# Performance work log

Measured on AMD Instinct MI355X. Metric: run time of the kernel, lower is better.

The kernel has to match this reference:

```python
import jax, jax.numpy as jnp
import numpy as np

B, F_, D, DIM, HEADS, DH = 1, 16, 576, 320, 8, 40
INNER = HEADS * DH          # 320
CROSS, TLEN = 768, 77
FF_INNER = 4 * DIM          # 1280
EPS = 1e-5


def _ln(x, w, b):
    mu = jnp.mean(x, axis=-1, keepdims=True)
    var = jnp.mean(jnp.square(x - mu), axis=-1, keepdims=True)
    return (x - mu) * jax.lax.rsqrt(var + EPS) * w + b


def _mha(q, k, v, heads):
    # q: [n, sq, inner], k/v: [n, sk, inner]
    n, sq, inner = q.shape
    sk = k.shape[1]
    dh = inner // heads
    q = q.reshape(n, sq, heads, dh).transpose(0, 2, 1, 3)
    k = k.reshape(n, sk, heads, dh).transpose(0, 2, 1, 3)
    v = v.reshape(n, sk, heads, dh).transpose(0, 2, 1, 3)
    scores = jnp.einsum('nhqd,nhkd->nhqk', q, k) * (dh ** -0.5)
    probs = jax.nn.softmax(scores, axis=-1)
    out = jnp.einsum('nhqk,nhkd->nhqd', probs, v)
    return out.transpose(0, 2, 1, 3).reshape(n, sq, inner)


def setup_inputs():
    key = jax.random.key(0)
    ks = jax.random.split(key, 32)
    s = 0.02

    def W(k, shape):
        return jax.random.normal(k, shape, jnp.float32) * s

    return {
        'hidden_states': jax.random.normal(ks[0], (B * F_, D, DIM), jnp.float32),
        'encoder_hidden_states': jax.random.normal(ks[1], (B * F_, TLEN, CROSS), jnp.float32),
        'ln1_w': jnp.ones((DIM,)), 'ln1_b': jnp.zeros((DIM,)),
        'q1_w': W(ks[2], (DIM, INNER)), 'k1_w': W(ks[3], (DIM, INNER)), 'v1_w': W(ks[4], (DIM, INNER)),
        'o1_w': W(ks[5], (INNER, DIM)), 'o1_b': jnp.zeros((DIM,)),
        'ln2_w': jnp.ones((DIM,)), 'ln2_b': jnp.zeros((DIM,)),
        'q2_w': W(ks[6], (DIM, INNER)), 'k2_w': W(ks[7], (CROSS, INNER)), 'v2_w': W(ks[8], (CROSS, INNER)),
        'o2_w': W(ks[9], (INNER, DIM)), 'o2_b': jnp.zeros((DIM,)),
        'lnt_w': jnp.ones((DIM,)), 'lnt_b': jnp.zeros((DIM,)),
        'qt_w': W(ks[10], (DIM, INNER)), 'kt_w': W(ks[11], (DIM, INNER)), 'vt_w': W(ks[12], (DIM, INNER)),
        'ot_w': W(ks[13], (INNER, DIM)), 'ot_b': jnp.zeros((DIM,)),
        'ln3_w': jnp.ones((DIM,)), 'ln3_b': jnp.zeros((DIM,)),
        'geglu_w': W(ks[14], (DIM, 2 * FF_INNER)), 'geglu_b': jnp.zeros((2 * FF_INNER,)),
        'ffo_w': W(ks[15], (FF_INNER, DIM)), 'ffo_b': jnp.zeros((DIM,)),
        'video_length': F_,
    }


def reference(hidden_states, encoder_hidden_states,
              ln1_w, ln1_b, q1_w, k1_w, v1_w, o1_w, o1_b,
              ln2_w, ln2_b, q2_w, k2_w, v2_w, o2_w, o2_b,
              lnt_w, lnt_b, qt_w, kt_w, vt_w, ot_w, ot_b,
              ln3_w, ln3_b, geglu_w, geglu_b, ffo_w, ffo_b,
              video_length):
    bf, d, c = hidden_states.shape
    f = video_length
    b = bf // f

    # ---- 1. sparse-causal self attention ----
    norm = _ln(hidden_states, ln1_w, ln1_b)
    q = norm @ q1_w
    k = (norm @ k1_w).reshape(b, f, d, INNER)
    v = (norm @ v1_w).reshape(b, f, d, INNER)
    former = jnp.clip(jnp.arange(f) - 1, 0, None)  # former_frame_index, [0,0,1,...]
    first = jnp.broadcast_to(k[:, :1], (b, f, d, INNER))
    k = jnp.concatenate([first, k[:, former]], axis=2).reshape(bf, 2 * d, INNER)
    firstv = jnp.broadcast_to(v[:, :1], (b, f, d, INNER))
    v = jnp.concatenate([firstv, v[:, former]], axis=2).reshape(bf, 2 * d, INNER)
    attn1 = _mha(q, k, v, HEADS) @ o1_w + o1_b
    hidden_states = attn1 + hidden_states

    # ---- 2. cross attention ----
    norm = _ln(hidden_states, ln2_w, ln2_b)
    attn2 = _mha(norm @ q2_w, encoder_hidden_states @ k2_w,
                 encoder_hidden_states @ v2_w, HEADS) @ o2_w + o2_b
    hidden_states = attn2 + hidden_states

    # ---- 3. temporal attention: (b f) d c -> (b d) f c ----
    ht = hidden_states.reshape(b, f, d, c).transpose(0, 2, 1, 3).reshape(b * d, f, c)
    norm = _ln(ht, lnt_w, lnt_b)
    attn_t = _mha(norm @ qt_w, norm @ kt_w, norm @ vt_w, HEADS) @ ot_w + ot_b
    ht = attn_t + ht
    hidden_states = ht.reshape(b, d, f, c).transpose(0, 2, 1, 3).reshape(bf, d, c)

    # ---- 4. GEGLU feed-forward ----
    norm = _ln(hidden_states, ln3_w, ln3_b)
    proj = norm @ geglu_w + geglu_b
    x1, gate = jnp.split(proj, 2, axis=-1)
    ff = (x1 * jax.nn.gelu(gate, approximate=False)) @ ffo_w + ffo_b
    return ff + hidden_states
```

## Files before the change

### kernel.cpp

```cpp
#include <hip/hip_runtime.h>
#include <hip/hip_bf16.h>
#include <math.h>

typedef unsigned short u16;
typedef unsigned int   u32;
typedef __attribute__((ext_vector_type(4))) float f32x4;
typedef __attribute__((ext_vector_type(8))) short bf8;
typedef __attribute__((ext_vector_type(4))) short bf4;

#define DEV __device__ __forceinline__

constexpr int FRAMES = 16, DTOK = 576, CDIM = 320, NHEAD = 8, DH = 40;
constexpr int TOKS = FRAMES * DTOK;
constexpr int TLEN = 77;
constexpr int FFI  = 1280;

constexpr int FP = 68;

DEV float b2f(u16 u) { union { u32 i; float f; } v; v.i = ((u32)u) << 16; return v.f; }
DEV u16 f2b(float f) {
  union { float f; u32 i; } v; v.f = f;
  return (u16)((v.i + 0x7fffu + ((v.i >> 16) & 1u)) >> 16);
}
DEV u32 cvtpk(float lo, float hi) {
  u32 r;
  asm("v_cvt_pk_bf16_f32 %0, %1, %2" : "=v"(r) : "v"(lo), "v"(hi));
  return r;
}

DEV bf8 ldfrag(const u16* p) {
  bf4 lo = *(const bf4*)p;
  bf4 hi = *(const bf4*)(p + 16);
  bf8 r;
  r[0]=lo[0]; r[1]=lo[1]; r[2]=lo[2]; r[3]=lo[3];
  r[4]=hi[0]; r[5]=hi[1]; r[6]=hi[2]; r[7]=hi[3];
  return r;
}

DEV f32x4 mfma16(bf8 a, bf8 b, f32x4 c) {
  return __builtin_amdgcn_mfma_f32_16x16x32_bf16(a, b, c, 0, 0, 0);
}

struct TD { const float* src; u16* dst; int K; int N; };
struct TPack { TD d[15]; };

__global__ __launch_bounds__(256) void tr_k(TPack p) {
  TD t = p.d[blockIdx.y];
  int total = t.K * t.N;
  for (int i = blockIdx.x * 256 + threadIdx.x; i < total; i += gridDim.x * 256) {
    int k = i / t.N, n = i % t.N;
    t.dst[(long)n * t.K + k] = f2b(t.src[i]);
  }
}

__global__ __launch_bounds__(256)
void ln_k(const float* __restrict__ X, const float* __restrict__ wt,
          const float* __restrict__ bs, u16* __restrict__ out) {
  const int row  = blockIdx.x * 4 + (threadIdx.x >> 6);
  const int lane = threadIdx.x & 63;
  const long base = (long)row * CDIM;
  float v[5];
#pragma unroll
  for (int i = 0; i < 5; i++) v[i] = X[base + i * 64 + lane];
  float s = v[0] + v[1] + v[2] + v[3] + v[4];
#pragma unroll
  for (int d = 1; d < 64; d <<= 1) s += __shfl_xor(s, d);
  const float mu = s * (1.0f / 320.0f);
  float dv[5], q = 0.f;
#pragma unroll
  for (int i = 0; i < 5; i++) { dv[i] = v[i] - mu; q += dv[i] * dv[i]; }
#pragma unroll
  for (int d = 1; d < 64; d <<= 1) q += __shfl_xor(q, d);
  const float rs = rsqrtf(q * (1.0f / 320.0f) + 1e-5f);
#pragma unroll
  for (int i = 0; i < 5; i++) {
    int c = i * 64 + lane;
    out[base + c] = f2b(dv[i] * rs * wt[c] + bs[c]);
  }
}

template<int MODE>
__global__ __launch_bounds__(256)
void gemm_k(const u16* __restrict__ A,
            const u16* __restrict__ Ba, const u16* __restrict__ Bb,
            const u16* __restrict__ Bc,
            u16* oa, u16* ob, u16* oc,
            const float* __restrict__ bias, const float* __restrict__ bias2,
            const float* __restrict__ resf, float* __restrict__ outf,
            int M, int N, int K, float oscale) {
  int bx, by, bz;
  {
    const int gx = gridDim.x, gy = gridDim.y, gz = gridDim.z;
    const int nwg = gx * gy * gz;
    int flat = blockIdx.x + gx * (blockIdx.y + gy * blockIdx.z);
    int orig = ((nwg & 7) == 0) ? (flat & 7) * (nwg >> 3) + (flat >> 3) : flat;
    bz = orig % gz;
    int rem = orig / gz;
    bx = rem % gx;
    by = rem / gx;
  }

  const u16* BT; u16* outb;
  if (MODE == 2) { BT = Ba; outb = oa; }
  else {
    BT   = (bz == 0) ? Ba : (bz == 1 ? Bb : Bc);
    outb = (bz == 0) ? oa : (bz == 1 ? ob : oc);
  }
  const u16* BT2 = Bb;
  const float zscale = (MODE == 0 && bz == 0) ? oscale : 1.0f;

  __shared__ __align__(16) u16 As[2][128][FP];
  __shared__ __align__(16) u16 Bs[2][64][FP];
  __shared__ __align__(16) u16 Bs2[(MODE == 2) ? 2 : 1][(MODE == 2) ? 64 : 1][(MODE == 2) ? FP : 1];

  const int tid = threadIdx.x;
  const int lane = tid & 63, w = tid >> 6;
  const int lr = lane & 15, lg = lane >> 4;
  const int wr = w >> 1, wc = w & 1;
  const long bm = (long)by * 128;
  const int  bn = bx * 64;

  f32x4 acc[4][2];
  f32x4 acc2[(MODE == 2) ? 4 : 1][(MODE == 2) ? 2 : 1];
  const f32x4 z4 = {0.f, 0.f, 0.f, 0.f};
#pragma unroll
  for (int f = 0; f < 4; f++)
#pragma unroll
    for (int g = 0; g < 2; g++) { acc[f][g] = z4; if (MODE == 2) acc2[f][g] = z4; }

  const int  arow = tid >> 1, aseg = tid & 1;
  const long agr  = bm + arow;
  const int  brow = tid >> 2, bseg = tid & 3;
  const bf8  zv   = {0,0,0,0,0,0,0,0};

  bf8 aReg[4], bReg[2], bReg2[(MODE == 2) ? 2 : 1];
  auto prefetch = [&](int k0) {
    const u16* asrc = A + agr * K + k0 + aseg * 32;
    if (agr < M) {
#pragma unroll
      for (int i = 0; i < 4; i++) aReg[i] = *(const bf8*)(asrc + i * 8);
    } else {
#pragma unroll
      for (int i = 0; i < 4; i++) aReg[i] = zv;
    }
    const u16* bsrc = BT + (long)(bn + brow) * K + k0 + bseg * 16;
    bReg[0] = *(const bf8*)(bsrc);
    bReg[1] = *(const bf8*)(bsrc + 8);
    if (MODE == 2) {
      const u16* bsrc2 = BT2 + (long)(bn + brow) * K + k0 + bseg * 16;
      bReg2[0] = *(const bf8*)(bsrc2);
      bReg2[1] = *(const bf8*)(bsrc2 + 8);
    }
  };
  auto writeLDS = [&](int buf) {
#pragma unroll
    for (int i = 0; i < 4; i++)
      *(bf8*)&As[buf][arow][aseg * 32 + i * 8] = aReg[i];
    *(bf8*)&Bs[buf][brow][bseg * 16]     = bReg[0];
    *(bf8*)&Bs[buf][brow][bseg * 16 + 8] = bReg[1];
    if (MODE == 2) {
      *(bf8*)&Bs2[buf][brow][bseg * 16]     = bReg2[0];
      *(bf8*)&Bs2[buf][brow][bseg * 16 + 8] = bReg2[1];
    }
  };

  prefetch(0);
  writeLDS(0);
  if (K > 64) prefetch(64);

  int cur = 0;
  for (int k0 = 0; k0 < K; k0 += 64) {
    asm volatile("s_waitcnt lgkmcnt(0)" ::: "memory");
    __builtin_amdgcn_s_barrier();

#pragma unroll
    for (int kk = 0; kk < 64; kk += 32) {
      bf8 af[4], bfr[2], bfr2[2];
#pragma unroll
      for (int f = 0; f < 4; f++)
        af[f] = ldfrag(&As[cur][wr * 64 + f * 16 + lr][kk + lg * 4]);
#pragma unroll
      for (int g = 0; g < 2; g++)
        bfr[g] = ldfrag(&Bs[cur][wc * 32 + g * 16 + lr][kk + lg * 4]);
      if (MODE == 2) {
#pragma unroll
        for (int g = 0; g < 2; g++)
          bfr2[g] = ldfrag(&Bs2[cur][wc * 32 + g * 16 + lr][kk + lg * 4]);
      }
#pragma unroll
      for (int f = 0; f < 4; f++)
#pragma unroll
        for (int g = 0; g < 2; g++) {
          acc[f][g] = mfma16(af[f], bfr[g], acc[f][g]);
          if (MODE == 2) acc2[f][g] = mfma16(af[f], bfr2[g], acc2[f][g]);
        }
    }

    if (k0 + 64 < K) {
      writeLDS(cur ^ 1);
      if (k0 + 128 < K) prefetch(k0 + 128);
    }
    cur ^= 1;
  }

#pragma unroll
  for (int f = 0; f < 4; f++)
#pragma unroll
    for (int g = 0; g < 2; g++)
#pragma unroll
      for (int j = 0; j < 4; j++) {
        long gm = bm + wr * 64 + f * 16 + lg * 4 + j;
        if (gm >= M) continue;
        int gn = bn + wc * 32 + g * 16 + lr;
        long o = gm * N + gn;
        float v = acc[f][g][j];
        if (MODE == 0) outb[o] = f2b(v * zscale);
        if (MODE == 1) outf[o] = v + bias[gn] + resf[o];
        if (MODE == 2) {
          float x1 = v + bias[gn];
          float gt = acc2[f][g][j] + bias2[gn];
          float ge = 0.5f * gt * (1.0f + erff(gt * 0.70710678118f));
          outb[o] = f2b(x1 * ge);
        }
      }
}

template<int MODE>
__global__ __launch_bounds__(256)
void flash_k(const u16* __restrict__ Q, const u16* __restrict__ Kb,
             const u16* __restrict__ Vb, u16* __restrict__ O) {
  __shared__ __align__(16) u16 Ks[2][64][FP];
  __shared__ __align__(16) u16 Vt[2][48][FP];
  u16 (*Qs)[FP] = Ks[1];

  int qb, h, n;
  {
    int flat = blockIdx.x + 9 * (blockIdx.y + 8 * blockIdx.z);
    int orig = (flat & 7) * 144 + (flat >> 3);
    qb = orig % 9; int rem = orig / 9;
    h = rem & 7; n = rem >> 3;
  }
  const int tid = threadIdx.x, lane = tid & 63, w = tid >> 6;
  const int lr = lane & 15, lg = lane >> 4;
  const int hoff = h * DH;

  constexpr int NCH   = (MODE == 0) ? 18 : 2;
  constexpr int KVLEN = (MODE == 0) ? 2 * DTOK : TLEN;
  const int nch = (MODE == 0 && n == 0) ? 9 : NCH;
  const int fprev = (n == 0) ? 0 : n - 1;
  const u16* Kh = Kb + hoff;
  const u16* Vh = Vb + hoff;

  int rS[5], cS[5]; long off[5];
#pragma unroll
  for (int j = 0; j < 5; j++) {
    int e = tid + j * 256;
    rS[j] = e / 20; cS[j] = (e % 20) * 2;
    off[j] = (long)rS[j] * CDIM + cS[j];
  }

  u32 kreg[5], vreg[5];
  auto prefetch = [&](int cc) {
    if (MODE == 0) {
      const long rowbase = (cc < 9) ? (long)cc * 64
                                    : (long)fprev * DTOK + (cc - 9) * 64;
      const u16* kp = Kh + rowbase * CDIM;
      const u16* vp = Vh + rowbase * CDIM;
#pragma unroll
      for (int j = 0; j < 5; j++) {
        kreg[j] = *(const u32*)(kp + off[j]);
        vreg[j] = *(const u32*)(vp + off[j]);
      }
    } else {
#pragma unroll
      for (int j = 0; j < 5; j++) {
        int t = cc * 64 + rS[j];
        bool valid = t < TLEN;
        long o = ((long)n * TLEN + t) * CDIM + cS[j];
        kreg[j] = valid ? *(const u32*)(Kh + o) : 0u;
        vreg[j] = valid ? *(const u32*)(Vh + o) : 0u;
      }
    }
  };
  auto writeKV = [&](int buf) {
#pragma unroll
    for (int j = 0; j < 5; j++) *(u32*)&Ks[buf][rS[j]][cS[j]] = kreg[j];
#pragma unroll
    for (int j = 0; j < 5; j++) {
      Vt[buf][cS[j]][rS[j]]     = (u16)(vreg[j] & 0xffffu);
      Vt[buf][cS[j] + 1][rS[j]] = (u16)(vreg[j] >> 16);
    }
  };

  prefetch(0);

  for (int i = tid; i < 64 * 24; i += 256) {
    int r = i / 24, c = 40 + (i % 24);
    Ks[0][r][c] = 0; Ks[1][r][c] = 0;
  }
  for (int i = tid; i < 8 * 64; i += 256) {
    int r = 40 + (i >> 6), c = i & 63;
    u16 pv = (r == 40) ? (u16)0x3F80 : (u16)0;
    Vt[0][r][c] = pv; Vt[1][r][c] = pv;
  }

  const int qrow0 = n * DTOK + qb * 64;
  for (int i = tid; i < 64 * 20; i += 256) {
    int r = i / 20, cp = (i % 20) * 2;
    *(u32*)&Qs[r][cp] = *(const u32*)(Q + (long)(qrow0 + r) * CDIM + hoff + cp);
  }
  writeKV(0);
  if (nch > 1) prefetch(1);
  asm volatile("s_waitcnt lgkmcnt(0)" ::: "memory");
  __builtin_amdgcn_s_barrier();

  bf8 qf[2];
  {
    const u16* p = &Qs[w * 16 + lr][0];
    qf[0] = ldfrag(p + lg * 4);
    qf[1] = ldfrag(p + 32 + lg * 4);
  }
  asm volatile("s_waitcnt lgkmcnt(0)" ::: "memory");
  __builtin_amdgcn_s_barrier();

  f32x4 oacc[3];
  const f32x4 z4 = {0.f, 0.f, 0.f, 0.f};
#pragma unroll
  for (int g = 0; g < 3; g++) oacc[g] = z4;

  int cur = 0;

  for (int cc = 0; cc < nch; cc++) {
    f32x4 s[4];
#pragma unroll
    for (int nf = 0; nf < 4; nf++) {
      const u16* kp = &Ks[cur][nf * 16 + lr][0];
      bf8 k0 = ldfrag(kp + lg * 4);
      bf8 k1 = ldfrag(kp + 32 + lg * 4);
      f32x4 z = z4;
      z = mfma16(k0, qf[0], z);
      z = mfma16(k1, qf[1], z);
      s[nf] = z;
    }

    float pvv[16];
#pragma unroll
    for (int nf = 0; nf < 4; nf++)
#pragma unroll
      for (int j = 0; j < 4; j++) {
        float p = exp2f(s[nf][j]);
        if (MODE == 1) {
          int kv = cc * 64 + nf * 16 + lg * 4 + j;
          if (kv >= KVLEN) p = 0.f;
        }
        pvv[nf * 4 + j] = p;
      }
    union { u32 u[4]; bf8 v; } P0, P1;
#pragma unroll
    for (int k2 = 0; k2 < 4; k2++) {
      P0.u[k2] = cvtpk(pvv[2 * k2],     pvv[2 * k2 + 1]);
      P1.u[k2] = cvtpk(pvv[8 + 2 * k2], pvv[8 + 2 * k2 + 1]);
    }
    bf8 pf0 = P0.v, pf1 = P1.v;

#pragma unroll
    for (int g = 0; g < 3; g++) {
      const u16* vp = &Vt[cur][g * 16 + lr][0];
      bf8 v0 = ldfrag(vp + lg * 4);
      bf8 v1 = ldfrag(vp + 32 + lg * 4);
      oacc[g] = mfma16(pf0, v0, oacc[g]);
      oacc[g] = mfma16(pf1, v1, oacc[g]);
    }

    if (cc + 1 < nch) {
      writeKV(cur ^ 1);
      if (cc + 2 < nch) prefetch(cc + 2);
      asm volatile("s_waitcnt lgkmcnt(0)" ::: "memory");
      __builtin_amdgcn_s_barrier();
    }
    cur ^= 1;
  }

  float lsum[4];
#pragma unroll
  for (int j = 0; j < 4; j++)
    lsum[j] = __shfl(oacc[2][j], (lane & 0x30) + 8);

#pragma unroll
  for (int g = 0; g < 3; g++) {
    int col = g * 16 + lr;
    if (col < DH) {
#pragma unroll
      for (int j = 0; j < 4; j++) {
        long row = qrow0 + w * 16 + lg * 4 + j;
        O[row * CDIM + hoff + col] = f2b(oacc[g][j] / lsum[j]);
      }
    }
  }
}

__global__ __launch_bounds__(64)
void tattn_k(const u16* __restrict__ Q, const u16* __restrict__ Kb,
             const u16* __restrict__ Vb, u16* __restrict__ O) {
  const int d = blockIdx.x, h = blockIdx.y;
  const int lane = threadIdx.x;
  __shared__ float Qs[16][41], Ks[16][41], Vs[16][41], Ps[16][17];
  const int hoff = h * DH;
#pragma unroll
  for (int i = 0; i < 10; i++) {
    int e = lane + 64 * i;
    int t = e / 40, c = e % 40;
    long src = (long)(t * DTOK + d) * CDIM + hoff + c;
    Qs[t][c] = b2f(Q[src]); Ks[t][c] = b2f(Kb[src]); Vs[t][c] = b2f(Vb[src]);
  }
  __syncthreads();
  const int ki = lane & 15, qg = lane >> 4;
  float p[4];
#pragma unroll
  for (int j = 0; j < 4; j++) {
    int qi = qg * 4 + j;
    float s = 0.f;
#pragma unroll
    for (int c = 0; c < 40; c++) s += Qs[qi][c] * Ks[ki][c];
    p[j] = s;
  }
#pragma unroll
  for (int j = 0; j < 4; j++) {
    float mx = p[j];
#pragma unroll
    for (int dd = 1; dd < 16; dd <<= 1) mx = fmaxf(mx, __shfl_xor(mx, dd));
    float e = exp2f(p[j] - mx);
    float ss = e;
#pragma unroll
    for (int dd = 1; dd < 16; dd <<= 1) ss += __shfl_xor(ss, dd);
    Ps[qg * 4 + j][ki] = e / ss;
  }
  __syncthreads();
  const int qi2 = lane & 15, dg = lane >> 4;
#pragma unroll
  for (int mI = 0; mI < 10; mI++) {
    int dd = dg * 10 + mI;
    float o = 0.f;
#pragma unroll
    for (int k2 = 0; k2 < 16; k2++) o += Ps[qi2][k2] * Vs[k2][dd];
    O[(long)(qi2 * DTOK + d) * CDIM + hoff + dd] = f2b(o);
  }
}

extern "C" void kernel_launch(void* const* d_in, const int* in_sizes, int n_in,
                              void* d_out, int out_size, void* d_ws, size_t ws_size,
                              hipStream_t stream) {
  const float* hid  = (const float*)d_in[0];
  const float* enc  = (const float*)d_in[1];
  const float* ln1w = (const float*)d_in[2];  const float* ln1b = (const float*)d_in[3];
  const float* q1w  = (const float*)d_in[4];  const float* k1w  = (const float*)d_in[5];
  const float* v1w  = (const float*)d_in[6];  const float* o1w  = (const float*)d_in[7];
  const float* o1b  = (const float*)d_in[8];
  const float* ln2w = (const float*)d_in[9];  const float* ln2b = (const float*)d_in[10];
  const float* q2w  = (const float*)d_in[11]; const float* k2w  = (const float*)d_in[12];
  const float* v2w  = (const float*)d_in[13]; const float* o2w  = (const float*)d_in[14];
  const float* o2b  = (const float*)d_in[15];
  const float* lntw = (const float*)d_in[16]; const float* lntb = (const float*)d_in[17];
  const float* qtw  = (const float*)d_in[18]; const float* ktw  = (const float*)d_in[19];
  const float* vtw  = (const float*)d_in[20]; const float* otw  = (const float*)d_in[21];
  const float* otb  = (const float*)d_in[22];
  const float* ln3w = (const float*)d_in[23]; const float* ln3b = (const float*)d_in[24];
  const float* gegw = (const float*)d_in[25]; const float* gegb = (const float*)d_in[26];
  const float* ffow = (const float*)d_in[27]; const float* ffob = (const float*)d_in[28];

  char* ws = (char*)d_ws;
  size_t off = 0;
  auto alloc = [&](size_t bytes) -> void* {
    void* p = ws + off;
    off = (off + bytes + 255) & ~(size_t)255;
    return p;
  };

  u16* wq1T = (u16*)alloc(320 * 320 * 2);
  u16* wk1T = (u16*)alloc(320 * 320 * 2);
  u16* wv1T = (u16*)alloc(320 * 320 * 2);
  u16* wo1T = (u16*)alloc(320 * 320 * 2);
  u16* wq2T = (u16*)alloc(320 * 320 * 2);
  u16* wk2T = (u16*)alloc(768 * 320 * 2);
  u16* wv2T = (u16*)alloc(768 * 320 * 2);
  u16* wo2T = (u16*)alloc(320 * 320 * 2);
  u16* wqtT = (u16*)alloc(320 * 320 * 2);
  u16* wktT = (u16*)alloc(320 * 320 * 2);
  u16* wvtT = (u16*)alloc(320 * 320 * 2);
  u16* wotT = (u16*)alloc(320 * 320 * 2);
  u16* wggT = (u16*)alloc(320 * 2560 * 2);
  u16* wfoT = (u16*)alloc(1280 * 320 * 2);

  u16*   ffin  = (u16*)alloc((size_t)TOKS * FFI * 2);
  u16* Qb    = ffin;
  u16* Kb    = ffin + (size_t)TOKS * CDIM;
  u16* Vb    = ffin + (size_t)2 * TOKS * CDIM;
  u16* attnB = ffin + (size_t)3 * TOKS * CDIM;
  u16*   normA = (u16*)alloc((size_t)TOKS * CDIM * 2);
  u16*   encB  = (u16*)alloc((size_t)16 * TLEN * 768 * 2);
  float* H1    = (float*)alloc((size_t)TOKS * CDIM * 4);
  float* H2    = (float*)alloc((size_t)TOKS * CDIM * 4);
  float* H3    = H1;

  if (off > ws_size) return;

  const int ENCN = 16 * TLEN * 768;
  TPack tp;
  tp.d[0]  = {q1w, wq1T, 320, 320};
  tp.d[1]  = {k1w, wk1T, 320, 320};
  tp.d[2]  = {v1w, wv1T, 320, 320};
  tp.d[3]  = {o1w, wo1T, 320, 320};
  tp.d[4]  = {q2w, wq2T, 320, 320};
  tp.d[5]  = {k2w, wk2T, 768, 320};
  tp.d[6]  = {v2w, wv2T, 768, 320};
  tp.d[7]  = {o2w, wo2T, 320, 320};
  tp.d[8]  = {qtw, wqtT, 320, 320};
  tp.d[9]  = {ktw, wktT, 320, 320};
  tp.d[10] = {vtw, wvtT, 320, 320};
  tp.d[11] = {otw, wotT, 320, 320};
  tp.d[12] = {gegw, wggT, 320, 2560};
  tp.d[13] = {ffow, wfoT, 1280, 320};
  tp.d[14] = {enc,  encB, 1, ENCN};

  const int MENC = 16 * TLEN;
  const float QS = 0.2281101122f;

  tr_k<<<dim3(320, 15), 256, 0, stream>>>(tp);

  ln_k<<<TOKS / 4, 256, 0, stream>>>(hid, ln1w, ln1b, normA);
  gemm_k<0><<<dim3(5, 72, 3), 256, 0, stream>>>(normA, wq1T, wk1T, wv1T,
      Qb, Kb, Vb, nullptr, nullptr, nullptr, nullptr, TOKS, 320, 320, QS);
  flash_k<0><<<dim3(9, 8, 16), 256, 0, stream>>>(Qb, Kb, Vb, attnB);
  gemm_k<1><<<dim3(5, 72, 1), 256, 0, stream>>>(attnB, wo1T, nullptr, nullptr,
      nullptr, nullptr, nullptr, o1b, nullptr, hid, H1, TOKS, 320, 320, 1.f);

  ln_k<<<TOKS / 4, 256, 0, stream>>>(H1, ln2w, ln2b, normA);
  gemm_k<0><<<dim3(5, 72, 1), 256, 0, stream>>>(normA, wq2T, nullptr, nullptr,
      Qb, nullptr, nullptr, nullptr, nullptr, nullptr, nullptr, TOKS, 320, 320, QS);
  gemm_k<0><<<dim3(5, 10, 2), 256, 0, stream>>>(encB, wk2T, wv2T, nullptr,
      Kb, Vb, nullptr, nullptr, nullptr, nullptr, nullptr, MENC, 320, 768, 1.f);
  flash_k<1><<<dim3(9, 8, 16), 256, 0, stream>>>(Qb, Kb, Vb, attnB);
  gemm_k<1><<<dim3(5, 72, 1), 256, 0, stream>>>(attnB, wo2T, nullptr, nullptr,
      nullptr, nullptr, nullptr, o2b, nullptr, H1, H2, TOKS, 320, 320, 1.f);

  ln_k<<<TOKS / 4, 256, 0, stream>>>(H2, lntw, lntb, normA);
  gemm_k<0><<<dim3(5, 72, 3), 256, 0, stream>>>(normA, wqtT, wktT, wvtT,
      Qb, Kb, Vb, nullptr, nullptr, nullptr, nullptr, TOKS, 320, 320, QS);
  tattn_k<<<dim3(576, 8), 64, 0, stream>>>(Qb, Kb, Vb, attnB);
  gemm_k<1><<<dim3(5, 72, 1), 256, 0, stream>>>(attnB, wotT, nullptr, nullptr,
      nullptr, nullptr, nullptr, otb, nullptr, H2, H3, TOKS, 320, 320, 1.f);

  ln_k<<<TOKS / 4, 256, 0, stream>>>(H3, ln3w, ln3b, normA);
  gemm_k<2><<<dim3(20, 72, 1), 256, 0, stream>>>(normA, wggT, wggT + 1280 * 320,
      nullptr, ffin, nullptr, nullptr, gegb, gegb + 1280, nullptr, nullptr,
      TOKS, 1280, 320, 1.f);
  gemm_k<1><<<dim3(5, 72, 1), 256, 0, stream>>>(ffin, wfoT, nullptr, nullptr,
      nullptr, nullptr, nullptr, ffob, nullptr, H3, (float*)d_out, TOKS, 320, 1280, 1.f);
}
```

Baseline: 290.7 us.

## Load K and Q fragments straight from global into registers in flash attention

Drops the shared-memory K buffer and the Q staging step. K fragments are now read from global memory straight into registers and double-buffered across a two-chunk unrolled loop, so the next chunk's K loads overlap the current chunk's MFMAs. Q fragments are loaded directly, with the padded tail zeroed in registers, which removes one barrier and the LDS writes for K. The cost is more VGPR pressure and narrow strided global reads. In cross-attention mode, K rows past the 77-token length are now read without a bounds guard and rely on masking, so the last batch item may read past the end of the buffer.

```diff
diff --git a/kernel.cpp b/kernel.cpp
--- a/kernel.cpp
+++ b/kernel.cpp
@@ -229,9 +229,7 @@
 __global__ __launch_bounds__(256)
 void flash_k(const u16* __restrict__ Q, const u16* __restrict__ Kb,
              const u16* __restrict__ Vb, u16* __restrict__ O) {
-  __shared__ __align__(16) u16 Ks[2][64][FP];
   __shared__ __align__(16) u16 Vt[2][48][FP];
-  u16 (*Qs)[FP] = Ks[1];
 
   int qb, h, n;
   {
@@ -259,32 +257,25 @@
     off[j] = (long)rS[j] * CDIM + cS[j];
   }
 
-  u32 kreg[5], vreg[5];
-  auto prefetch = [&](int cc) {
+  u32 vreg[5];
+  auto prefetchV = [&](int cc) {
     if (MODE == 0) {
       const long rowbase = (cc < 9) ? (long)cc * 64
                                     : (long)fprev * DTOK + (cc - 9) * 64;
-      const u16* kp = Kh + rowbase * CDIM;
       const u16* vp = Vh + rowbase * CDIM;
 #pragma unroll
-      for (int j = 0; j < 5; j++) {
-        kreg[j] = *(const u32*)(kp + off[j]);
-        vreg[j] = *(const u32*)(vp + off[j]);
-      }
+      for (int j = 0; j < 5; j++) vreg[j] = *(const u32*)(vp + off[j]);
     } else {
 #pragma unroll
       for (int j = 0; j < 5; j++) {
         int t = cc * 64 + rS[j];
         bool valid = t < TLEN;
         long o = ((long)n * TLEN + t) * CDIM + cS[j];
-        kreg[j] = valid ? *(const u32*)(Kh + o) : 0u;
         vreg[j] = valid ? *(const u32*)(Vh + o) : 0u;
       }
     }
   };
-  auto writeKV = [&](int buf) {
-#pragma unroll
-    for (int j = 0; j < 5; j++) *(u32*)&Ks[buf][rS[j]][cS[j]] = kreg[j];
+  auto writeV = [&](int buf) {
 #pragma unroll
     for (int j = 0; j < 5; j++) {
       Vt[buf][cS[j]][rS[j]]     = (u16)(vreg[j] & 0xffffu);
@@ -292,100 +283,108 @@
     }
   };
 
-  prefetch(0);
-
-  for (int i = tid; i < 64 * 24; i += 256) {
-    int r = i / 24, c = 40 + (i % 24);
-    Ks[0][r][c] = 0; Ks[1][r][c] = 0;
-  }
+  auto loadK = [&](int cc, bf8 (&k0)[4], bf8 (&k1)[4]) {
+    long rowbase;
+    if (MODE == 0)
+      rowbase = (cc < 9) ? (long)cc * 64 : (long)fprev * DTOK + (cc - 9) * 64;
+    else
+      rowbase = (long)n * TLEN + cc * 64;
+#pragma unroll
+    for (int nf = 0; nf < 4; nf++) {
+      const u16* kp = Kh + (rowbase + nf * 16 + lr) * CDIM + lg * 4;
+      k0[nf] = ldfrag(kp);
+      k1[nf] = ldfrag(kp + 32);
+    }
+  };
+
+  bf8 kA0[4], kA1[4], kB0[4], kB1[4];
+
+  prefetchV(0);
+  loadK(0, kA0, kA1);
+
+  bf8 qf0, qf1;
+  {
+    const u16* qp = Q + (long)(n * DTOK + qb * 64 + w * 16 + lr) * CDIM + hoff + lg * 4;
+    qf0 = ldfrag(qp);
+    bf4 lo = (lg < 2) ? *(const bf4*)(qp + 32) : bf4{0, 0, 0, 0};
+    qf1[0] = lo[0]; qf1[1] = lo[1]; qf1[2] = lo[2]; qf1[3] = lo[3];
+    qf1[4] = 0; qf1[5] = 0; qf1[6] = 0; qf1[7] = 0;
+  }
+
   for (int i = tid; i < 8 * 64; i += 256) {
     int r = 40 + (i >> 6), c = i & 63;
     u16 pv = (r == 40) ? (u16)0x3F80 : (u16)0;
     Vt[0][r][c] = pv; Vt[1][r][c] = pv;
   }
 
-  const int qrow0 = n * DTOK + qb * 64;
-  for (int i = tid; i < 64 * 20; i += 256) {
-    int r = i / 20, cp = (i % 20) * 2;
-    *(u32*)&Qs[r][cp] = *(const u32*)(Q + (long)(qrow0 + r) * CDIM + hoff + cp);
-  }
-  writeKV(0);
-  if (nch > 1) prefetch(1);
+  writeV(0);
+  if (nch > 1) prefetchV(1);
   asm volatile("s_waitcnt lgkmcnt(0)" ::: "memory");
   __builtin_amdgcn_s_barrier();
 
-  bf8 qf[2];
-  {
-    const u16* p = &Qs[w * 16 + lr][0];
-    qf[0] = ldfrag(p + lg * 4);
-    qf[1] = ldfrag(p + 32 + lg * 4);
-  }
-  asm volatile("s_waitcnt lgkmcnt(0)" ::: "memory");
-  __builtin_amdgcn_s_barrier();
-
   f32x4 oacc[3];
   const f32x4 z4 = {0.f, 0.f, 0.f, 0.f};
 #pragma unroll
   for (int g = 0; g < 3; g++) oacc[g] = z4;
 
-  int cur = 0;
-
-  for (int cc = 0; cc < nch; cc++) {
-    f32x4 s[4];
-#pragma unroll
-    for (int nf = 0; nf < 4; nf++) {
-      const u16* kp = &Ks[cur][nf * 16 + lr][0];
-      bf8 k0 = ldfrag(kp + lg * 4);
-      bf8 k1 = ldfrag(kp + 32 + lg * 4);
-      f32x4 z = z4;
-      z = mfma16(k0, qf[0], z);
-      z = mfma16(k1, qf[1], z);
-      s[nf] = z;
-    }
-
-    float pvv[16];
-#pragma unroll
-    for (int nf = 0; nf < 4; nf++)
-#pragma unroll
-      for (int j = 0; j < 4; j++) {
-        float p = exp2f(s[nf][j]);
-        if (MODE == 1) {
-          int kv = cc * 64 + nf * 16 + lg * 4 + j;
-          if (kv >= KVLEN) p = 0.f;
-        }
-        pvv[nf * 4 + j] = p;
-      }
-    union { u32 u[4]; bf8 v; } P0, P1;
-#pragma unroll
-    for (int k2 = 0; k2 < 4; k2++) {
-      P0.u[k2] = cvtpk(pvv[2 * k2],     pvv[2 * k2 + 1]);
-      P1.u[k2] = cvtpk(pvv[8 + 2 * k2], pvv[8 + 2 * k2 + 1]);
-    }
-    bf8 pf0 = P0.v, pf1 = P1.v;
-
-#pragma unroll
-    for (int g = 0; g < 3; g++) {
-      const u16* vp = &Vt[cur][g * 16 + lr][0];
-      bf8 v0 = ldfrag(vp + lg * 4);
-      bf8 v1 = ldfrag(vp + 32 + lg * 4);
-      oacc[g] = mfma16(pf0, v0, oacc[g]);
-      oacc[g] = mfma16(pf1, v1, oacc[g]);
-    }
-
-    if (cc + 1 < nch) {
-      writeKV(cur ^ 1);
-      if (cc + 2 < nch) prefetch(cc + 2);
-      asm volatile("s_waitcnt lgkmcnt(0)" ::: "memory");
-      __builtin_amdgcn_s_barrier();
-    }
-    cur ^= 1;
-  }
+#define CHUNK_BODY(CC, K0, K1, KN0, KN1, VB)                                  \
+  {                                                                           \
+    const int cc_ = (CC);                                                     \
+    if (cc_ + 1 < nch) loadK(cc_ + 1, KN0, KN1);                              \
+    f32x4 s[4];                                                               \
+    _Pragma("unroll")                                                         \
+    for (int nf = 0; nf < 4; nf++) {                                          \
+      f32x4 z = z4;                                                           \
+      z = mfma16(K0[nf], qf0, z);                                             \
+      z = mfma16(K1[nf], qf1, z);                                             \
+      s[nf] = z;                                                              \
+    }                                                                         \
+    float pvv[16];                                                            \
+    _Pragma("unroll")                                                         \
+    for (int nf = 0; nf < 4; nf++)                                            \
+      _Pragma("unroll")                                                       \
+      for (int j = 0; j < 4; j++) {                                           \
+        float p = exp2f(s[nf][j]);                                            \
+        if (MODE == 1) {                                                      \
+          int kv = cc_ * 64 + nf * 16 + lg * 4 + j;                           \
+          if (kv >= KVLEN) p = 0.f;                                           \
+        }                                                                     \
+        pvv[nf * 4 + j] = p;                                                  \
+      }                                                                       \
+    union { u32 u[4]; bf8 v; } P0, P1;                                        \
+    _Pragma("unroll")                                                         \
+    for (int k2 = 0; k2 < 4; k2++) {                                          \
+      P0.u[k2] = cvtpk(pvv[2 * k2],     pvv[2 * k2 + 1]);                     \
+      P1.u[k2] = cvtpk(pvv[8 + 2 * k2], pvv[8 + 2 * k2 + 1]);                 \
+    }                                                                         \
+    _Pragma("unroll")                                                         \
+    for (int g = 0; g < 3; g++) {                                             \
+      const u16* vp = &Vt[VB][g * 16 + lr][0];                                \
+      bf8 v0 = ldfrag(vp + lg * 4);                                           \
+      bf8 v1 = ldfrag(vp + 32 + lg * 4);                                      \
+      oacc[g] = mfma16(P0.v, v0, oacc[g]);                                    \
+      oacc[g] = mfma16(P1.v, v1, oacc[g]);                                    \
+    }                                                                         \
+    if (cc_ + 1 < nch) {                                                      \
+      writeV(VB ^ 1);                                                         \
+      if (cc_ + 2 < nch) prefetchV(cc_ + 2);                                  \
+      asm volatile("s_waitcnt lgkmcnt(0)" ::: "memory");                      \
+      __builtin_amdgcn_s_barrier();                                           \
+    }                                                                         \
+  }
+
+  for (int cc = 0; cc < nch; cc += 2) {
+    CHUNK_BODY(cc, kA0, kA1, kB0, kB1, 0)
+    if (cc + 1 < nch) CHUNK_BODY(cc + 1, kB0, kB1, kA0, kA1, 1)
+  }
+#undef CHUNK_BODY
 
   float lsum[4];
 #pragma unroll
   for (int j = 0; j < 4; j++)
     lsum[j] = __shfl(oacc[2][j], (lane & 0x30) + 8);
 
+  const int qrow0 = n * DTOK + qb * 64;
 #pragma unroll
   for (int g = 0; g < 3; g++) {
     int col = g * 16 + lr;
```

New measurement: 417.2 us. +43.5%, slower.
